# Performance work log

Measured on AMD Instinct MI355X. Metric: run time of the kernel, lower is better.

The kernel has to match this reference:

```python
import jax, jax.numpy as jnp
import numpy as np

# ---- module constants (from init_kwargs / zounds.SR22050) ----
SEQ = 64
N_SAMPLES = 16384
N_EVENTS = 16
N_HARM = 32
NOISE_WS = 512
NOISE_STEP = 256
NYQ = 11025.0  # SR22050 nyquist
MIN_F0 = 20.0 / NYQ
MAX_F0 = 800.0 / NYQ
F0_DIFF = MAX_F0 - MIN_F0
HARM_FACTOR = jnp.arange(2, 2 + N_HARM, dtype=jnp.float32)  # [2..33]


def lin_interp(x, size):
    """torch F.interpolate(mode='linear', align_corners=False) along last dim."""
    L = x.shape[-1]
    pos = (jnp.arange(size, dtype=x.dtype) + 0.5) * (L / size) - 0.5
    pos = jnp.clip(pos, 0.0, L - 1)
    i0 = jnp.floor(pos).astype(jnp.int32)
    i1 = jnp.minimum(i0 + 1, L - 1)
    w = (pos - i0).astype(x.dtype)
    return x[..., i0] * (1.0 - w) + x[..., i1] * w


def band_filtered_noise(noise_frames, mean, std):
    """Per-frame Gaussian band-pass of white noise in the STFT domain, overlap-add.
    noise_frames: (b,e,F,ws); mean/std: (b,e,F) in normalized freq [0,1]."""
    ws = noise_frames.shape[-1]
    n = jnp.arange(ws, dtype=noise_frames.dtype)
    win = 0.5 - 0.5 * jnp.cos(2.0 * jnp.pi * n / ws)  # Hann
    spec = jnp.fft.rfft(noise_frames * win, axis=-1)  # (b,e,F,ws//2+1)
    freqs = jnp.linspace(0.0, 1.0, ws // 2 + 1)
    filt = jnp.exp(-0.5 * ((freqs[None, None, None, :] - mean[..., None]) / std[..., None]) ** 2)
    frames = jnp.fft.irfft(spec * filt, n=ws, axis=-1)  # (b,e,F,ws)
    # overlap-add with hop NOISE_STEP (ws == 2*step -> two half-chunks per frame)
    b, e, Fn, _ = frames.shape
    chunks = frames.reshape(b, e, Fn, 2, NOISE_STEP)
    a = chunks[..., 0, :].reshape(b, e, Fn * NOISE_STEP)
    c = chunks[..., 1, :].reshape(b, e, Fn * NOISE_STEP)
    out = jnp.zeros((b, e, (Fn + 1) * NOISE_STEP), dtype=frames.dtype)
    out = out.at[..., : Fn * NOISE_STEP].add(a)
    out = out.at[..., NOISE_STEP:].add(c)
    return out[..., :N_SAMPLES]


def setup_inputs() -> dict:
    key = jax.random.key(0)
    ks = jax.random.split(key, 8)
    B = 8
    return {
        "f0": jax.random.uniform(ks[0], (B, N_EVENTS, SEQ), jnp.float32),
        "overall_env": jax.random.uniform(ks[1], (B, N_EVENTS, SEQ), jnp.float32),
        "osc_env": jax.random.uniform(ks[2], (B, N_EVENTS, SEQ), jnp.float32),
        "noise_env": jax.random.uniform(ks[3], (B, N_EVENTS, SEQ), jnp.float32),
        "harm_env": jax.random.uniform(ks[4], (B, N_EVENTS, N_HARM, SEQ), jnp.float32),
        "noise_std": jax.random.uniform(ks[5], (B, N_EVENTS, SEQ), jnp.float32),
        "f0_baselines": jax.random.uniform(ks[6], (B, N_EVENTS, 1), jnp.float32),
        "noise_frames": jax.random.normal(ks[7], (B, N_EVENTS, SEQ, NOISE_WS), jnp.float32),
    }


def reference(f0, overall_env, osc_env, noise_env, harm_env, noise_std, f0_baselines, noise_frames):
    # f0_baselines branch (ERB-scaled deviation around baseline)
    f0 = jnp.clip(f0, -0.5, 0.5)
    scaled_erb = (0.108 * (f0_baselines * NYQ) + 24.7) / NYQ
    f0 = f0_baselines + f0 * scaled_erb

    orig_f0 = f0 = jnp.clip(f0, 0.0, 1.0)
    overall_env = jnp.clip(overall_env, 0.0, 1.0)
    osc_env = jnp.clip(osc_env, 0.0, 1.0)
    harm_env = jnp.clip(harm_env, 0.0, 1.0)
    noise_std = jnp.clip(noise_std, 1e-12, 1.0)

    f0n = MIN_F0 + f0 * F0_DIFF                                   # (b,e,S)
    harm_f = f0n[:, :, None, :] * HARM_FACTOR[None, None, :, None]  # (b,e,H,S)
    harm_env = osc_env[:, :, None, :] * harm_env                  # (b,e,H,S)

    fund = lin_interp(f0n, N_SAMPLES)           # (b,e,N)
    harm_f_i = lin_interp(harm_f, N_SAMPLES)    # (b,e,H,N)
    osc_env_i = lin_interp(osc_env, N_SAMPLES)  # (b,e,N)
    harm_env_i = lin_interp(harm_env, N_SAMPLES)

    fundamental = jnp.sin(jnp.cumsum(fund * jnp.pi, axis=-1)) * osc_env_i
    harmonics = (jnp.sin(jnp.cumsum(harm_f_i * jnp.pi, axis=-1)) * harm_env_i).sum(axis=-2)
    osc = fundamental + harmonics

    noise_mean = MIN_F0 + orig_f0 * F0_DIFF
    nstd = noise_std * F0_DIFF
    noise = band_filtered_noise(noise_frames, noise_mean, nstd)

    osc_mix = lin_interp(overall_env, N_SAMPLES)
    noise_mix = lin_interp(1.0 - overall_env, N_SAMPLES)
    return osc * osc_mix + noise * noise_mix
```

## Files before the change

kernel.cpp:

```cpp
#include <hip/hip_runtime.h>
#include <math.h>

#define SEQ 64
#define NSAMP 16384
#define NHARM 32
#define NWS 512
#define NSTEP 256
#define BE 128
#define NFRAMES 8192

typedef _Float16 half8 __attribute__((ext_vector_type(8)));
typedef float f32x4 __attribute__((ext_vector_type(4)));

__device__ __forceinline__ float sin_rev(float x) {
  float r; asm("v_sin_f32 %0, %1" : "=v"(r) : "v"(x)); return r;
}
__device__ __forceinline__ float cos_rev(float x) {
  float r; asm("v_cos_f32 %0, %1" : "=v"(r) : "v"(x)); return r;
}
__device__ __forceinline__ float clip01(float v) { return fminf(fmaxf(v, 0.0f), 1.0f); }

__device__ __forceinline__ float f0_to_norm(float f0v, float bl) {
  const float NYQ = 11025.0f;
  const float MIN_F0 = 20.0f / 11025.0f;
  const float F0_DIFF = 780.0f / 11025.0f;
  float v = fminf(fmaxf(f0v, -0.5f), 0.5f);
  float erb = (0.108f * (bl * NYQ) + 24.7f) / NYQ;
  float fv = clip01(bl + v * erb);
  return MIN_F0 + fv * F0_DIFF;
}

__global__ __launch_bounds__(256) void gemmf_k(const float* __restrict__ Af,
                                               _Float16* __restrict__ Cout,
                                               _Float16* __restrict__ W2,
                                               const float* __restrict__ f0,
                                               const float* __restrict__ nstd,
                                               const float* __restrict__ f0b) {
  const int tid = threadIdx.x;

  if (blockIdx.x < 256) {
    const int k = tid & 127;
    const bool isSin = tid >= 128;
#pragma unroll
    for (int rr = 0; rr < 2; ++rr) {
      const int n = blockIdx.x * 2 + rr;
      int a = (k * n) & 511;
      float ph = (float)a * (1.0f / 512.0f);
      W2[n * 256 + tid] = (_Float16)(isSin ? sin_rev(ph) : cos_rev(ph));
    }
    return;
  }

  const int p = blockIdx.x - 256;
  const int x = p & 7, j = p >> 3;
  const int mstripe = ((j >> 2) << 3) + x;
  const int bn0 = (j & 3) * 64;
  const int m0 = mstripe * 32;

  const int Kt = 512;
  const int wave = tid >> 6, lane = tid & 63;
  const int r = lane & 15, q = lane >> 4;
  const int wr = (wave & 1) * 16;
  const int wc = (wave >> 1) * 32;
  __shared__ __align__(16) _Float16 Ash[2][32 * 64];
  __shared__ __align__(16) _Float16 Bsh[2][64 * 64];
  __shared__ __align__(16) float whann[512];

  const int nT = Kt >> 6;
  const int srowA = tid >> 3;
  const int srowB0 = tid >> 3, srowB1 = (256 + tid) >> 3;
  const int skg = tid & 7;

  half8 ra, rb[2];
  f32x4 acc[2] = {};

  whann[tid] = 0.5f - 0.5f * cos_rev((float)tid * (1.0f / 512.0f));
  whann[tid + 256] = 0.5f - 0.5f * cos_rev((float)(tid + 256) * (1.0f / 512.0f));
  __syncthreads();

  const int kB0 = (bn0 + srowB0) & 127;
  const int kB1 = (bn0 + srowB1) & 127;
  const bool sB0 = (bn0 + srowB0) >= 128;
  const bool sB1 = (bn0 + srowB1) >= 128;

  auto load_a = [&](int kk) {
    const float* s0 = Af + (size_t)(m0 + srowA) * Kt + kk + skg * 8;
    float4 a0 = ((const float4*)s0)[0], a1 = ((const float4*)s0)[1];
    float4 w0 = *(const float4*)(&whann[kk + skg * 8]);
    float4 w1 = *(const float4*)(&whann[kk + skg * 8 + 4]);
    ra[0] = (_Float16)(a0.x * w0.x); ra[1] = (_Float16)(a0.y * w0.y);
    ra[2] = (_Float16)(a0.z * w0.z); ra[3] = (_Float16)(a0.w * w0.w);
    ra[4] = (_Float16)(a1.x * w1.x); ra[5] = (_Float16)(a1.y * w1.y);
    ra[6] = (_Float16)(a1.z * w1.z); ra[7] = (_Float16)(a1.w * w1.w);
  };
  auto gen_b = [&](int kk) {
    const int nbase = kk + skg * 8;
#pragma unroll
    for (int jj = 0; jj < 8; ++jj) {
      const int n = nbase + jj;
      float ph0 = (float)((kB0 * n) & 511) * (1.0f / 512.0f);
      float ph1 = (float)((kB1 * n) & 511) * (1.0f / 512.0f);
      rb[0][jj] = (_Float16)(sB0 ? sin_rev(ph0) : cos_rev(ph0));
      rb[1][jj] = (_Float16)(sB1 ? sin_rev(ph1) : cos_rev(ph1));
    }
  };
  auto store_lds = [&](int b) {
    *(half8*)(&Ash[b][srowA * 64 + ((skg ^ (srowA & 7)) << 3)]) = ra;
    *(half8*)(&Bsh[b][srowB0 * 64 + ((skg ^ (srowB0 & 7)) << 3)]) = rb[0];
    *(half8*)(&Bsh[b][srowB1 * 64 + ((skg ^ (srowB1 & 7)) << 3)]) = rb[1];
  };

  load_a(0);
  gen_b(0);
  store_lds(0);

  for (int t = 0;;) {
    if (t + 1 < nT) { load_a((t + 1) << 6); gen_b((t + 1) << 6); }
    __syncthreads();
    const int b = t & 1;
#pragma unroll
    for (int ks = 0; ks < 2; ++ks) {
      const int kg = ks * 4 + q;
      const int ar = wr + r;
      half8 af = *(const half8*)(&Ash[b][ar * 64 + ((kg ^ (ar & 7)) << 3)]);
#pragma unroll
      for (int ni = 0; ni < 2; ++ni) {
        const int br = wc + ni * 16 + r;
        half8 bf = *(const half8*)(&Bsh[b][br * 64 + ((kg ^ (br & 7)) << 3)]);
        acc[ni] = __builtin_amdgcn_mfma_f32_16x16x32_f16(af, bf, acc[ni], 0, 0, 0);
      }
    }
    if (t + 1 >= nT) break;
    __syncthreads();
    store_lds((t + 1) & 1);
    ++t;
  }

  const float F0_DIFF = 780.0f / 11025.0f;
#pragma unroll
  for (int reg = 0; reg < 4; ++reg) {
    const int row = m0 + wr + q * 4 + reg;
    const float mu = f0_to_norm(f0[row], f0b[row >> 6]);
    const float sd = fminf(fmaxf(nstd[row], 1e-12f), 1.0f) * F0_DIFF;
    const float inv_sd = 1.0f / sd;
    const float a = inv_sd * (1.0f / 256.0f);
    const float bmu = mu * inv_sd;
#pragma unroll
    for (int ni = 0; ni < 2; ++ni) {
      const int col = bn0 + wc + ni * 16 + r;
      const int k = col & 127;
      float z = fmaf((float)k, a, -bmu);
      float cf = (k == 0) ? (1.0f / 512.0f) : (2.0f / 512.0f);
      float s = cf * exp2f(z * z * -0.72134752044f);
      Cout[(size_t)row * 256 + col] = (_Float16)(acc[ni][reg] * s);
    }
  }
}

__global__ __launch_bounds__(256) void invfin_k(const _Float16* __restrict__ AB,
                                                const _Float16* __restrict__ W2,
                                                const float* __restrict__ f0,
                                                const float* __restrict__ f0b,
                                                const float* __restrict__ oenv_g,
                                                const float* __restrict__ oscenv_g,
                                                const float* __restrict__ henv_g,
                                                float* __restrict__ out) {
  const int p = blockIdx.x;
  const int x = p & 7, j = p >> 3;
  const int be = ((j >> 3) << 3) + x;
  const int sub = j & 7;
  const int chalf = sub >> 2;
  const int n0 = (sub & 3) * 64;
  const int m0c = be * 64 + chalf * 32;
  const int tid = threadIdx.x;
  const int wave = tid >> 6, lane = tid & 63;
  const int r = lane & 15, q = lane >> 4;
  const int wr = (wave & 1) * 16;
  const int wc = (wave >> 1) * 32;

  __shared__ __align__(16) _Float16 A2sh[33 * 64];
  __shared__ __align__(16) _Float16 B1sh[64 * 64];
  __shared__ __align__(16) _Float16 B2sh[64 * 64];
  __shared__ __align__(16) float4 qe4[8 * SEQ];
  __shared__ float oenv[SEQ], oscE[SEQ];
  __shared__ float Fs[SEQ], Ds[SEQ], Gs[SEQ];

  if (tid < SEQ) {
    oenv[tid] = clip01(oenv_g[be * SEQ + tid]);
    oscE[tid] = clip01(oscenv_g[be * SEQ + tid]);
    Fs[tid] = f0_to_norm(f0[be * SEQ + tid], f0b[be]);
  }
  __syncthreads();

  if (tid < SEQ) {
    const int s = tid;
    float fcur = Fs[s];
    float fnxt = (s < 63) ? Fs[s + 1] : Fs[63];
    Ds[s] = fnxt - fcur;
    double term = 128.0 * ((double)fcur + (double)fnxt);
    double sc = term;
#pragma unroll
    for (int off = 1; off < 64; off <<= 1) {
      double u = __shfl_up(sc, off, 64);
      if (s >= off) sc += u;
    }
    double C = 128.0 * (double)Fs[0] + (sc - term);
    Gs[s] = (float)(C - 2.0 * floor(C * 0.5));
  }

  for (int idx = tid; idx < 8 * SEQ; idx += 256) {
    int hq = idx >> 6, s = idx & 63;
    const float* hb = henv_g + (size_t)be * (NHARM * SEQ) + (4 * hq) * SEQ + s;
    float e = oscE[s];
    qe4[idx] = make_float4(e * clip01(hb[0]), e * clip01(hb[64]),
                           e * clip01(hb[128]), e * clip01(hb[192]));
  }

  half8 raA0, raA1, rbB[4];
  const int rowA0 = tid >> 3, kgA0 = tid & 7;
  const int rowA1 = (256 + tid) >> 3, kgA1 = tid & 7;

  auto stage_load = [&](int kk) {
    {
      half8 v = {0, 0, 0, 0, 0, 0, 0, 0};
      if (rowA0 > 0 || chalf == 1)
        v = *(const half8*)(AB + (size_t)(m0c - 1 + rowA0) * 256 + kk + kgA0 * 8);
      raA0 = v;
    }
    if (tid < 8)
      raA1 = *(const half8*)(AB + (size_t)(m0c - 1 + rowA1) * 256 + kk + kgA1 * 8);
#pragma unroll
    for (int it = 0; it < 4; ++it) {
      int g = it * 256 + tid;
      int row = (g >> 3) & 63;
      bool second = g >= 512;
      int wrow = n0 + row + (second ? 256 : 0);
      rbB[it] = *(const half8*)(W2 + (size_t)wrow * 256 + kk + (g & 7) * 8);
    }
  };
  auto stage_write = [&]() {
    *(half8*)(&A2sh[rowA0 * 64 + ((kgA0 ^ (rowA0 & 7)) << 3)]) = raA0;
    if (tid < 8)
      *(half8*)(&A2sh[rowA1 * 64 + ((kgA1 ^ (rowA1 & 7)) << 3)]) = raA1;
#pragma unroll
    for (int it = 0; it < 4; ++it) {
      int g = it * 256 + tid;
      int row = (g >> 3) & 63;
      _Float16* dst = (g >= 512) ? B2sh : B1sh;
      *(half8*)(&dst[row * 64 + (((g & 7) ^ (row & 7)) << 3)]) = rbB[it];
    }
  };

  f32x4 acc[2] = {};
  stage_load(0);
  stage_write();
  __syncthreads();

  for (int t = 0;;) {
    if (t < 3) stage_load((t + 1) << 6);
#pragma unroll
    for (int ks = 0; ks < 2; ++ks) {
      const int kg = ks * 4 + q;
      const int ra1 = 1 + wr + r;
      const int ra2 = wr + r;
      half8 af1 = *(const half8*)(&A2sh[ra1 * 64 + ((kg ^ (ra1 & 7)) << 3)]);
      half8 af2 = *(const half8*)(&A2sh[ra2 * 64 + ((kg ^ (ra2 & 7)) << 3)]);
#pragma unroll
      for (int ni = 0; ni < 2; ++ni) {
        const int rb = wc + ni * 16 + r;
        const int sw = (kg ^ (rb & 7)) << 3;
        half8 bf1 = *(const half8*)(&B1sh[rb * 64 + sw]);
        half8 bf2 = *(const half8*)(&B2sh[rb * 64 + sw]);
        acc[ni] = __builtin_amdgcn_mfma_f32_16x16x32_f16(af1, bf1, acc[ni], 0, 0, 0);
        acc[ni] = __builtin_amdgcn_mfma_f32_16x16x32_f16(af2, bf2, acc[ni], 0, 0, 0);
      }
    }
    if (t == 3) break;
    __syncthreads();
    stage_write();
    __syncthreads();
    ++t;
  }

#pragma unroll
  for (int reg = 0; reg < 4; ++reg) {
    const int c = chalf * 32 + wr + q * 4 + reg;
#pragma unroll
    for (int ni = 0; ni < 2; ++ni) {
      const int n = n0 + wc + ni * 16 + r;
      const int t = c * 256 + n;
      float pos = ((float)t + 0.5f) * (1.0f / 256.0f) - 0.5f;
      pos = fminf(fmaxf(pos, 0.0f), 63.0f);
      int i0 = (int)pos;
      int i1 = min(i0 + 1, 63);
      float w = pos - (float)i0;

      float pph;
      if (t < 128) {
        pph = (float)(t + 1) * Fs[0];
      } else {
        int s = (t - 128) >> 8;
        float u1 = (float)((t - 128) - (s << 8) + 1);
        pph = Gs[s] + fmaf(Ds[s] * (1.0f / 512.0f), u1 * u1, u1 * Fs[s]);
      }
      pph = pph - 2.0f * floorf(pph * 0.5f);
      float xv = pph * 0.5f;
      float sb = sin_rev(xv);
      float cb = cos_rev(xv);
      float C = 2.0f * cb;

      float fund = sb * (oscE[i0] * (1.0f - w) + oscE[i1] * w);
      float d0 = 0.0f, d1 = 0.0f;
      float sp = sb;
      float scur = C * sb;
#pragma unroll
      for (int hq = 0; hq < 8; ++hq) {
        float4 qa = qe4[hq * 64 + i0];
        float4 qb = qe4[hq * 64 + i1];
        d0 = fmaf(scur, qa.x, d0); d1 = fmaf(scur, qb.x, d1);
        sp = fmaf(C, scur, -sp);
        d0 = fmaf(sp, qa.y, d0);   d1 = fmaf(sp, qb.y, d1);
        scur = fmaf(C, sp, -scur);
        d0 = fmaf(scur, qa.z, d0); d1 = fmaf(scur, qb.z, d1);
        sp = fmaf(C, scur, -sp);
        d0 = fmaf(sp, qa.w, d0);   d1 = fmaf(sp, qb.w, d1);
        scur = fmaf(C, sp, -scur);
      }
      float osc = fund + d0 * (1.0f - w) + d1 * w;
      float mix = oenv[i0] * (1.0f - w) + oenv[i1] * w;
      out[(size_t)be * NSAMP + t] = fmaf(osc, mix, acc[ni][reg] * (1.0f - mix));
    }
  }
}

extern "C" void kernel_launch(void* const* d_in, const int* in_sizes, int n_in,
                              void* d_out, int out_size, void* d_ws, size_t ws_size,
                              hipStream_t stream) {
  const float* f0           = (const float*)d_in[0];
  const float* overall_env  = (const float*)d_in[1];
  const float* osc_env      = (const float*)d_in[2];
  const float* harm_env     = (const float*)d_in[4];
  const float* noise_std    = (const float*)d_in[5];
  const float* f0_base      = (const float*)d_in[6];
  const float* noise_frames = (const float*)d_in[7];
  float* out = (float*)d_out;

  _Float16* W2 = (_Float16*)d_ws;
  _Float16* AB = W2 + 512 * 256;

  gemmf_k<<<1280, 256, 0, stream>>>(noise_frames, AB, W2, f0, noise_std, f0_base);
  invfin_k<<<1024, 256, 0, stream>>>(
      AB, W2, f0, f0_base, overall_env, osc_env, harm_env, out);
}
```

Before: 33.53 us.

## Fuse forward and inverse DFT kernels with per-stripe atomic flag synchronization

```diff
diff --git a/kernel.cpp b/kernel.cpp
--- a/kernel.cpp
+++ b/kernel.cpp
@@ -30,160 +30,146 @@
   return MIN_F0 + fv * F0_DIFF;
 }
 
-__global__ __launch_bounds__(256) void gemmf_k(const float* __restrict__ Af,
-                                               _Float16* __restrict__ Cout,
-                                               _Float16* __restrict__ W2,
-                                               const float* __restrict__ f0,
-                                               const float* __restrict__ nstd,
-                                               const float* __restrict__ f0b) {
+__global__ __launch_bounds__(256, 4) void fused_k(
+    const float* __restrict__ Af,
+    const float* __restrict__ f0,
+    const float* __restrict__ nstd,
+    const float* __restrict__ f0b,
+    const float* __restrict__ oenv_g,
+    const float* __restrict__ oscenv_g,
+    const float* __restrict__ henv_g,
+    _Float16* __restrict__ AB,
+    unsigned int* __restrict__ flags,
+    float* __restrict__ out) {
+  __shared__ __align__(16) unsigned char smem[30464];
+  const int p = blockIdx.x;
   const int tid = threadIdx.x;
-
-  if (blockIdx.x < 256) {
-    const int k = tid & 127;
-    const bool isSin = tid >= 128;
-#pragma unroll
-    for (int rr = 0; rr < 2; ++rr) {
-      const int n = blockIdx.x * 2 + rr;
-      int a = (k * n) & 511;
-      float ph = (float)a * (1.0f / 512.0f);
-      W2[n * 256 + tid] = (_Float16)(isSin ? sin_rev(ph) : cos_rev(ph));
-    }
-    return;
-  }
-
-  const int p = blockIdx.x - 256;
   const int x = p & 7, j = p >> 3;
   const int mstripe = ((j >> 2) << 3) + x;
   const int bn0 = (j & 3) * 64;
   const int m0 = mstripe * 32;
-
-  const int Kt = 512;
   const int wave = tid >> 6, lane = tid & 63;
   const int r = lane & 15, q = lane >> 4;
   const int wr = (wave & 1) * 16;
   const int wc = (wave >> 1) * 32;
-  __shared__ __align__(16) _Float16 Ash[2][32 * 64];
-  __shared__ __align__(16) _Float16 Bsh[2][64 * 64];
-  __shared__ __align__(16) float whann[512];
-
-  const int nT = Kt >> 6;
-  const int srowA = tid >> 3;
-  const int srowB0 = tid >> 3, srowB1 = (256 + tid) >> 3;
-  const int skg = tid & 7;
-
-  half8 ra, rb[2];
-  f32x4 acc[2] = {};
-
-  whann[tid] = 0.5f - 0.5f * cos_rev((float)tid * (1.0f / 512.0f));
-  whann[tid + 256] = 0.5f - 0.5f * cos_rev((float)(tid + 256) * (1.0f / 512.0f));
+
+  {
+    _Float16* Ash = (_Float16*)smem;
+    _Float16* Bsh = (_Float16*)(smem + 8192);
+    float* whann = (float*)(smem + 24576);
+
+    const int Kt = 512;
+    const int nT = 8;
+    const int srowA = tid >> 3;
+    const int srowB0 = tid >> 3, srowB1 = (256 + tid) >> 3;
+    const int skg = tid & 7;
+
+    half8 ra, rb[2];
+    f32x4 acc[2] = {};
+
+    whann[tid] = 0.5f - 0.5f * cos_rev((float)tid * (1.0f / 512.0f));
+    whann[tid + 256] = 0.5f - 0.5f * cos_rev((float)(tid + 256) * (1.0f / 512.0f));
+    __syncthreads();
+
+    const int kB0 = (bn0 + srowB0) & 127;
+    const int kB1 = (bn0 + srowB1) & 127;
+    const bool sB0 = (bn0 + srowB0) >= 128;
+    const bool sB1 = (bn0 + srowB1) >= 128;
+
+    auto load_a = [&](int kk) {
+      const float* s0 = Af + (size_t)(m0 + srowA) * Kt + kk + skg * 8;
+      float4 a0 = ((const float4*)s0)[0], a1 = ((const float4*)s0)[1];
+      float4 w0 = *(const float4*)(&whann[kk + skg * 8]);
+      float4 w1 = *(const float4*)(&whann[kk + skg * 8 + 4]);
+      ra[0] = (_Float16)(a0.x * w0.x); ra[1] = (_Float16)(a0.y * w0.y);
+      ra[2] = (_Float16)(a0.z * w0.z); ra[3] = (_Float16)(a0.w * w0.w);
+      ra[4] = (_Float16)(a1.x * w1.x); ra[5] = (_Float16)(a1.y * w1.y);
+      ra[6] = (_Float16)(a1.z * w1.z); ra[7] = (_Float16)(a1.w * w1.w);
+    };
+    auto gen_b = [&](int kk) {
+      const int nbase = kk + skg * 8;
+#pragma unroll
+      for (int jj = 0; jj < 8; ++jj) {
+        const int n = nbase + jj;
+        float ph0 = (float)((kB0 * n) & 511) * (1.0f / 512.0f);
+        float ph1 = (float)((kB1 * n) & 511) * (1.0f / 512.0f);
+        rb[0][jj] = (_Float16)(sB0 ? sin_rev(ph0) : cos_rev(ph0));
+        rb[1][jj] = (_Float16)(sB1 ? sin_rev(ph1) : cos_rev(ph1));
+      }
+    };
+    auto store_lds = [&](int b) {
+      *(half8*)(&Ash[b * 2048 + srowA * 64 + ((skg ^ (srowA & 7)) << 3)]) = ra;
+      *(half8*)(&Bsh[b * 4096 + srowB0 * 64 + ((skg ^ (srowB0 & 7)) << 3)]) = rb[0];
+      *(half8*)(&Bsh[b * 4096 + srowB1 * 64 + ((skg ^ (srowB1 & 7)) << 3)]) = rb[1];
+    };
+
+    load_a(0);
+    gen_b(0);
+    store_lds(0);
+
+    for (int t = 0;;) {
+      if (t + 1 < nT) { load_a((t + 1) << 6); gen_b((t + 1) << 6); }
+      __syncthreads();
+      const int b = t & 1;
+#pragma unroll
+      for (int ks = 0; ks < 2; ++ks) {
+        const int kg = ks * 4 + q;
+        const int ar = wr + r;
+        half8 af = *(const half8*)(&Ash[b * 2048 + ar * 64 + ((kg ^ (ar & 7)) << 3)]);
+#pragma unroll
+        for (int ni = 0; ni < 2; ++ni) {
+          const int br = wc + ni * 16 + r;
+          half8 bf = *(const half8*)(&Bsh[b * 4096 + br * 64 + ((kg ^ (br & 7)) << 3)]);
+          acc[ni] = __builtin_amdgcn_mfma_f32_16x16x32_f16(af, bf, acc[ni], 0, 0, 0);
+        }
+      }
+      if (t + 1 >= nT) break;
+      __syncthreads();
+      store_lds((t + 1) & 1);
+      ++t;
+    }
+
+    const float F0_DIFF = 780.0f / 11025.0f;
+#pragma unroll
+    for (int reg = 0; reg < 4; ++reg) {
+      const int row = m0 + wr + q * 4 + reg;
+      const float mu = f0_to_norm(f0[row], f0b[row >> 6]);
+      const float sd = fminf(fmaxf(nstd[row], 1e-12f), 1.0f) * F0_DIFF;
+      const float inv_sd = 1.0f / sd;
+      const float a = inv_sd * (1.0f / 256.0f);
+      const float bmu = mu * inv_sd;
+#pragma unroll
+      for (int ni = 0; ni < 2; ++ni) {
+        const int col = bn0 + wc + ni * 16 + r;
+        const int k = col & 127;
+        float z = fmaf((float)k, a, -bmu);
+        float cf = (k == 0) ? (1.0f / 512.0f) : (2.0f / 512.0f);
+        float s = cf * exp2f(z * z * -0.72134752044f);
+        AB[(size_t)row * 256 + col] = (_Float16)(acc[ni][reg] * s);
+      }
+    }
+  }
+
   __syncthreads();
-
-  const int kB0 = (bn0 + srowB0) & 127;
-  const int kB1 = (bn0 + srowB1) & 127;
-  const bool sB0 = (bn0 + srowB0) >= 128;
-  const bool sB1 = (bn0 + srowB1) >= 128;
-
-  auto load_a = [&](int kk) {
-    const float* s0 = Af + (size_t)(m0 + srowA) * Kt + kk + skg * 8;
-    float4 a0 = ((const float4*)s0)[0], a1 = ((const float4*)s0)[1];
-    float4 w0 = *(const float4*)(&whann[kk + skg * 8]);
-    float4 w1 = *(const float4*)(&whann[kk + skg * 8 + 4]);
-    ra[0] = (_Float16)(a0.x * w0.x); ra[1] = (_Float16)(a0.y * w0.y);
-    ra[2] = (_Float16)(a0.z * w0.z); ra[3] = (_Float16)(a0.w * w0.w);
-    ra[4] = (_Float16)(a1.x * w1.x); ra[5] = (_Float16)(a1.y * w1.y);
-    ra[6] = (_Float16)(a1.z * w1.z); ra[7] = (_Float16)(a1.w * w1.w);
-  };
-  auto gen_b = [&](int kk) {
-    const int nbase = kk + skg * 8;
-#pragma unroll
-    for (int jj = 0; jj < 8; ++jj) {
-      const int n = nbase + jj;
-      float ph0 = (float)((kB0 * n) & 511) * (1.0f / 512.0f);
-      float ph1 = (float)((kB1 * n) & 511) * (1.0f / 512.0f);
-      rb[0][jj] = (_Float16)(sB0 ? sin_rev(ph0) : cos_rev(ph0));
-      rb[1][jj] = (_Float16)(sB1 ? sin_rev(ph1) : cos_rev(ph1));
-    }
-  };
-  auto store_lds = [&](int b) {
-    *(half8*)(&Ash[b][srowA * 64 + ((skg ^ (srowA & 7)) << 3)]) = ra;
-    *(half8*)(&Bsh[b][srowB0 * 64 + ((skg ^ (srowB0 & 7)) << 3)]) = rb[0];
-    *(half8*)(&Bsh[b][srowB1 * 64 + ((skg ^ (srowB1 & 7)) << 3)]) = rb[1];
-  };
-
-  load_a(0);
-  gen_b(0);
-  store_lds(0);
-
-  for (int t = 0;;) {
-    if (t + 1 < nT) { load_a((t + 1) << 6); gen_b((t + 1) << 6); }
-    __syncthreads();
-    const int b = t & 1;
-#pragma unroll
-    for (int ks = 0; ks < 2; ++ks) {
-      const int kg = ks * 4 + q;
-      const int ar = wr + r;
-      half8 af = *(const half8*)(&Ash[b][ar * 64 + ((kg ^ (ar & 7)) << 3)]);
-#pragma unroll
-      for (int ni = 0; ni < 2; ++ni) {
-        const int br = wc + ni * 16 + r;
-        half8 bf = *(const half8*)(&Bsh[b][br * 64 + ((kg ^ (br & 7)) << 3)]);
-        acc[ni] = __builtin_amdgcn_mfma_f32_16x16x32_f16(af, bf, acc[ni], 0, 0, 0);
-      }
-    }
-    if (t + 1 >= nT) break;
-    __syncthreads();
-    store_lds((t + 1) & 1);
-    ++t;
-  }
-
-  const float F0_DIFF = 780.0f / 11025.0f;
-#pragma unroll
-  for (int reg = 0; reg < 4; ++reg) {
-    const int row = m0 + wr + q * 4 + reg;
-    const float mu = f0_to_norm(f0[row], f0b[row >> 6]);
-    const float sd = fminf(fmaxf(nstd[row], 1e-12f), 1.0f) * F0_DIFF;
-    const float inv_sd = 1.0f / sd;
-    const float a = inv_sd * (1.0f / 256.0f);
-    const float bmu = mu * inv_sd;
-#pragma unroll
-    for (int ni = 0; ni < 2; ++ni) {
-      const int col = bn0 + wc + ni * 16 + r;
-      const int k = col & 127;
-      float z = fmaf((float)k, a, -bmu);
-      float cf = (k == 0) ? (1.0f / 512.0f) : (2.0f / 512.0f);
-      float s = cf * exp2f(z * z * -0.72134752044f);
-      Cout[(size_t)row * 256 + col] = (_Float16)(acc[ni][reg] * s);
-    }
-  }
-}
-
-__global__ __launch_bounds__(256) void invfin_k(const _Float16* __restrict__ AB,
-                                                const _Float16* __restrict__ W2,
-                                                const float* __restrict__ f0,
-                                                const float* __restrict__ f0b,
-                                                const float* __restrict__ oenv_g,
-                                                const float* __restrict__ oscenv_g,
-                                                const float* __restrict__ henv_g,
-                                                float* __restrict__ out) {
-  const int p = blockIdx.x;
-  const int x = p & 7, j = p >> 3;
-  const int be = ((j >> 3) << 3) + x;
-  const int sub = j & 7;
-  const int chalf = sub >> 2;
-  const int n0 = (sub & 3) * 64;
-  const int m0c = be * 64 + chalf * 32;
-  const int tid = threadIdx.x;
-  const int wave = tid >> 6, lane = tid & 63;
-  const int r = lane & 15, q = lane >> 4;
-  const int wr = (wave & 1) * 16;
-  const int wc = (wave >> 1) * 32;
-
-  __shared__ __align__(16) _Float16 A2sh[33 * 64];
-  __shared__ __align__(16) _Float16 B1sh[64 * 64];
-  __shared__ __align__(16) _Float16 B2sh[64 * 64];
-  __shared__ __align__(16) float4 qe4[8 * SEQ];
-  __shared__ float oenv[SEQ], oscE[SEQ];
-  __shared__ float Fs[SEQ], Ds[SEQ], Gs[SEQ];
+  if (tid == 0) {
+    __threadfence();
+    __hip_atomic_fetch_add(&flags[mstripe], 1u, __ATOMIC_ACQ_REL,
+                           __HIP_MEMORY_SCOPE_AGENT);
+  }
+
+  const int be = mstripe >> 1;
+  const int chalf = mstripe & 1;
+  const int n0c = bn0;
+
+  _Float16* A2sh = (_Float16*)smem;
+  _Float16* B1sh = (_Float16*)(smem + 4224);
+  _Float16* B2sh = (_Float16*)(smem + 12416);
+  float4* qe4 = (float4*)(smem + 20608);
+  float* oenv = (float*)(smem + 28800);
+  float* oscE = (float*)(smem + 29056);
+  float* Fs = (float*)(smem + 29312);
+  float* Ds = (float*)(smem + 29568);
+  float* Gs = (float*)(smem + 29824);
 
   if (tid < SEQ) {
     oenv[tid] = clip01(oenv_g[be * SEQ + tid]);
@@ -218,30 +204,32 @@
 
   half8 raA0, raA1, rbB[4];
   const int rowA0 = tid >> 3, kgA0 = tid & 7;
-  const int rowA1 = (256 + tid) >> 3, kgA1 = tid & 7;
-
-  auto stage_load = [&](int kk) {
-    {
-      half8 v = {0, 0, 0, 0, 0, 0, 0, 0};
-      if (rowA0 > 0 || chalf == 1)
-        v = *(const half8*)(AB + (size_t)(m0c - 1 + rowA0) * 256 + kk + kgA0 * 8);
-      raA0 = v;
-    }
-    if (tid < 8)
-      raA1 = *(const half8*)(AB + (size_t)(m0c - 1 + rowA1) * 256 + kk + kgA1 * 8);
+  const int rowA1 = (256 + tid) >> 3;
+
+  auto gen_w2 = [&](int kk) {
 #pragma unroll
     for (int it = 0; it < 4; ++it) {
       int g = it * 256 + tid;
       int row = (g >> 3) & 63;
-      bool second = g >= 512;
-      int wrow = n0 + row + (second ? 256 : 0);
-      rbB[it] = *(const half8*)(W2 + (size_t)wrow * 256 + kk + (g & 7) * 8);
+      int n = n0c + row + ((g >= 512) ? 256 : 0);
+#pragma unroll
+      for (int jj = 0; jj < 8; ++jj) {
+        int kap = kk + (g & 7) * 8 + jj;
+        int k = kap & 127;
+        float ph = (float)((k * n) & 511) * (1.0f / 512.0f);
+        rbB[it][jj] = (_Float16)((kap >= 128) ? sin_rev(ph) : cos_rev(ph));
+      }
     }
   };
-  auto stage_write = [&]() {
-    *(half8*)(&A2sh[rowA0 * 64 + ((kgA0 ^ (rowA0 & 7)) << 3)]) = raA0;
+  auto load_a2 = [&](int kk) {
+    half8 v = {0, 0, 0, 0, 0, 0, 0, 0};
+    if (rowA0 > 0 || chalf == 1)
+      v = *(const half8*)(AB + (size_t)(m0 - 1 + rowA0) * 256 + kk + kgA0 * 8);
+    raA0 = v;
     if (tid < 8)
-      *(half8*)(&A2sh[rowA1 * 64 + ((kgA1 ^ (rowA1 & 7)) << 3)]) = raA1;
+      raA1 = *(const half8*)(AB + (size_t)(m0 - 1 + rowA1) * 256 + kk + kgA0 * 8);
+  };
+  auto write_b = [&]() {
 #pragma unroll
     for (int it = 0; it < 4; ++it) {
       int g = it * 256 + tid;
@@ -250,14 +238,33 @@
       *(half8*)(&dst[row * 64 + (((g & 7) ^ (row & 7)) << 3)]) = rbB[it];
     }
   };
+  auto write_a = [&]() {
+    *(half8*)(&A2sh[rowA0 * 64 + ((kgA0 ^ (rowA0 & 7)) << 3)]) = raA0;
+    if (tid < 8)
+      *(half8*)(&A2sh[rowA1 * 64 + ((kgA0 ^ (rowA1 & 7)) << 3)]) = raA1;
+  };
+
+  gen_w2(0);
+  write_b();
+
+  if (tid == 0) {
+    while (__hip_atomic_load(&flags[mstripe], __ATOMIC_ACQUIRE,
+                             __HIP_MEMORY_SCOPE_AGENT) < 4u)
+      __builtin_amdgcn_s_sleep(4);
+    if (chalf)
+      while (__hip_atomic_load(&flags[mstripe - 1], __ATOMIC_ACQUIRE,
+                               __HIP_MEMORY_SCOPE_AGENT) < 4u)
+        __builtin_amdgcn_s_sleep(4);
+  }
+  __syncthreads();
 
   f32x4 acc[2] = {};
-  stage_load(0);
-  stage_write();
+  load_a2(0);
+  write_a();
   __syncthreads();
 
   for (int t = 0;;) {
-    if (t < 3) stage_load((t + 1) << 6);
+    if (t < 3) { load_a2((t + 1) << 6); gen_w2((t + 1) << 6); }
 #pragma unroll
     for (int ks = 0; ks < 2; ++ks) {
       const int kg = ks * 4 + q;
@@ -277,7 +284,8 @@
     }
     if (t == 3) break;
     __syncthreads();
-    stage_write();
+    write_a();
+    write_b();
     __syncthreads();
     ++t;
   }
@@ -287,7 +295,7 @@
     const int c = chalf * 32 + wr + q * 4 + reg;
 #pragma unroll
     for (int ni = 0; ni < 2; ++ni) {
-      const int n = n0 + wc + ni * 16 + r;
+      const int n = n0c + wc + ni * 16 + r;
       const int t = c * 256 + n;
       float pos = ((float)t + 0.5f) * (1.0f / 256.0f) - 0.5f;
       pos = fminf(fmaxf(pos, 0.0f), 63.0f);
@@ -345,10 +353,12 @@
   const float* noise_frames = (const float*)d_in[7];
   float* out = (float*)d_out;
 
-  _Float16* W2 = (_Float16*)d_ws;
-  _Float16* AB = W2 + 512 * 256;
-
-  gemmf_k<<<1280, 256, 0, stream>>>(noise_frames, AB, W2, f0, noise_std, f0_base);
-  invfin_k<<<1024, 256, 0, stream>>>(
-      AB, W2, f0, f0_base, overall_env, osc_env, harm_env, out);
-}
+  _Float16* AB = (_Float16*)d_ws;
+  unsigned int* flags = (unsigned int*)(AB + (size_t)NFRAMES * 256);
+
+  hipMemsetAsync(flags, 0, 256 * sizeof(unsigned int), stream);
+
+  fused_k<<<1024, 256, 0, stream>>>(
+      noise_frames, f0, noise_std, f0_base, overall_env, osc_env, harm_env,
+      AB, flags, out);
+}
```

Measured after the change: 103.6 us. +208.9%, slower.
